# Kernel tuning notes

Hardware: AMD Instinct MI355X
Metric: run time of the kernel (lower is better)

Reference implementation:

```python
import jax, jax.numpy as jnp
import numpy as np

D_MODEL = 256
N_LAYERS = 8
NUM_CLASSES = 3
INPUT_DIM = 1
BATCH = 8
SEQ = 2048
EXIT_IDX = (1, 3, 5, 7)  # n_layers//4-1, n_layers//2-1, 3n//4-1, n-1
LN_EPS = 1e-5


def setup_inputs() -> dict:
    key = jax.random.key(0)
    ks = jax.random.split(key, 16)
    d, nl, nc = D_MODEL, N_LAYERS, NUM_CLASSES
    return {
        "x": jax.random.normal(ks[0], (BATCH, SEQ, INPUT_DIM), jnp.float32),
        "in_W": jax.random.normal(ks[1], (d, INPUT_DIM), jnp.float32) * 0.02,
        "in_b": jnp.zeros((d,), jnp.float32),
        "A_params": jax.random.normal(ks[2], (nl, d), jnp.float32) * 0.1,
        "B_params": jax.random.normal(ks[3], (nl, d), jnp.float32),
        "C_params": jax.random.normal(ks[4], (nl, d), jnp.float32),
        "D_params": jax.random.normal(ks[5], (nl, d), jnp.float32),
        "proj_W": jax.random.normal(ks[6], (nl, d, d), jnp.float32) * 0.02,
        "proj_b": jnp.zeros((nl, d), jnp.float32),
        "ln_g": jnp.ones((nl, d), jnp.float32),
        "ln_b": jnp.zeros((nl, d), jnp.float32),
        "head_W": jax.random.normal(ks[7], (4, nc, d), jnp.float32) * 0.02,
        "head_b": jnp.zeros((4, nc), jnp.float32),
    }


def _ssm_block(x, Ap, Bp, Cp, Dp, pW, pb, g, b):
    # x: [B, L, d]
    Bsz, L, d = x.shape
    A = jax.nn.sigmoid(Ap)                               # [d]
    t = jnp.arange(L, dtype=jnp.float32)
    K = (Cp[:, None] * (A[:, None] ** t[None, :]) * Bp[:, None])[:, None, :]  # [d,1,L]
    xt = jnp.swapaxes(x, 1, 2)                           # [B, d, L]
    # torch F.conv1d(pad=L-1, groups=d) then [..., :L] == left-pad-only cross-correlation
    out = jax.lax.conv_general_dilated(
        xt, K, window_strides=(1,), padding=[(L - 1, 0)], feature_group_count=d
    )                                                    # [B, d, L]
    out = out + Dp[None, :, None] * xt
    out = jnp.swapaxes(out, 1, 2)                        # [B, L, d]
    out = jax.nn.gelu(out, approximate=False) @ pW.T + pb
    y = x + out
    mu = jnp.mean(y, axis=-1, keepdims=True)
    var = jnp.var(y, axis=-1, keepdims=True)
    return (y - mu) / jnp.sqrt(var + LN_EPS) * g + b


def reference(x, in_W, in_b, A_params, B_params, C_params, D_params,
              proj_W, proj_b, ln_g, ln_b, head_W, head_b):
    h = x @ in_W.T + in_b                                # [B, L, d]
    logits = []
    head = 0
    for i in range(N_LAYERS):
        h = _ssm_block(h, A_params[i], B_params[i], C_params[i], D_params[i],
                       proj_W[i], proj_b[i], ln_g[i], ln_b[i])
        if i in EXIT_IDX:
            pooled = jnp.mean(h, axis=1)                 # [B, d]
            logits.append(pooled @ head_W[head].T + head_b[head])
            head += 1
    return jnp.stack(logits, axis=0)                     # [4, B, num_classes]
```

## Files before the change

kernel.cpp:

```cpp
#include <hip/hip_runtime.h>
#include <math.h>

#define DM 256
#define LSEQ 2048
#define BATCH 8
#define NLAYER 8
#define EMAX 192
#define LN_EPS 1e-5f
#define BM 32
#define BLKS 64
#define NPROD 7
#define TAILB 57

#define AL_OFF  16384
#define RED_OFF 32768
#define SMEM_SZ (RED_OFF + 1280)

typedef float f32x4 __attribute__((ext_vector_type(4)));
typedef short bf16x8 __attribute__((ext_vector_type(8)));
typedef unsigned short u16;
typedef unsigned short u16x4 __attribute__((ext_vector_type(4)));
typedef unsigned short u16x8 __attribute__((ext_vector_type(8)));

union V8 { u16x8 u; bf16x8 b; };

__device__ __forceinline__ float erf_fast(float x) {
    float ax = fabsf(x);
    float t = __builtin_amdgcn_rcpf(fmaf(0.3275911f, ax, 1.f));
    float p = fmaf(t, 1.061405429f, -1.453152027f);
    p = fmaf(t, p, 1.421413741f);
    p = fmaf(t, p, -0.284496736f);
    p = fmaf(t, p, 0.254829592f);
    p = p * t;
    float e = __expf(-ax * ax);
    float r = 1.f - p * e;
    return copysignf(r, x);
}

__device__ __forceinline__ float gelu_fast(float v) {
    return 0.5f * v * (1.f + erf_fast(v * 0.70710678118654752f));
}

__device__ __forceinline__ void split2(float g, u16& hi, u16& lo) {
    unsigned u = __float_as_uint(g);
    hi = (u16)(u >> 16);
    float fh = __uint_as_float(u & 0xFFFF0000u);
    float r = g - fh;
    unsigned v = __float_as_uint(r);
    v = v + 0x7FFFu + ((v >> 16) & 1u);
    lo = (u16)(v >> 16);
}

__device__ __forceinline__ int a_addr(int row, int wn, int fr) {
    int unit = wn * 8 + (fr >> 1);
    return row * 512 + ((unit ^ (row & 7)) << 4) + (fr & 1) * 8;
}

__global__ void k_prep(const float* __restrict__ pW, u16* __restrict__ pWh,
                       u16* __restrict__ pWl,
                       const float* __restrict__ x, const float* __restrict__ inW,
                       const float* __restrict__ inb, const float* __restrict__ Ap,
                       const float* __restrict__ Bp, const float* __restrict__ Cp,
                       float* __restrict__ P_all, float* __restrict__ logA_all,
                       float* __restrict__ CB_all, float* __restrict__ pooled,
                       int* __restrict__ flags) {
    if (blockIdx.x < 256) {
        int i = blockIdx.x * 256 + threadIdx.x;
        int e = i * 8;
        int l = e >> 16;
        int r = e & 65535;
        int cg = r >> 12;
        int ks = (r >> 9) & 7;
        int lane = (r >> 3) & 63;
        int fq = lane >> 4, fr = lane & 15;
        int col = (cg >> 2) * 64 + fr * 4 + (cg & 3);
        int k = ks * 32 + fq * 8;
        const float* src = pW + l * 65536 + col * 256 + k;
        float4 w0 = *(const float4*)src;
        float4 w1 = *(const float4*)(src + 4);
        float vv[8] = {w0.x, w0.y, w0.z, w0.w, w1.x, w1.y, w1.z, w1.w};
        u16 sh[8], sl[8];
#pragma unroll
        for (int j = 0; j < 8; ++j) split2(vv[j], sh[j], sl[j]);
        u16x8 vh = {sh[0], sh[1], sh[2], sh[3], sh[4], sh[5], sh[6], sh[7]};
        u16x8 vl = {sl[0], sl[1], sl[2], sl[3], sl[4], sl[5], sl[6], sl[7]};
        *(u16x8*)&pWh[e] = vh;
        *(u16x8*)&pWl[e] = vl;
    } else {
        int b = blockIdx.x - 256;
        int c = threadIdx.x;
        float A0 = 1.f / (1.f + expf(-Ap[c]));
        float iw = inW[c], ib = inb[c];
        const float* xb = x + b * LSEQ;
        float pw = 1.f, acc = 0.f;
        for (int t = 0; t <= EMAX; ++t) {
            acc += (xb[t] * iw + ib) * pw;
            pw *= A0;
        }
        P_all[b * DM + c] = acc;
        for (int l = 1; l < NLAYER; ++l) P_all[l * BATCH * DM + b * DM + c] = 0.f;
        for (int e = 0; e < 4; ++e) pooled[e * BATCH * DM + b * DM + c] = 0.f;
        if (b == 0) {
            for (int l = 0; l < NLAYER; ++l) {
                float Al = 1.f / (1.f + expf(-Ap[l * DM + c]));
                logA_all[l * DM + c] = logf(Al);
                CB_all[l * DM + c]   = Bp[l * DM + c] * Cp[l * DM + c];
            }
            if (c < NLAYER * BATCH) flags[c] = 0;
        }
    }
}

__global__ __launch_bounds__(256, 1) void k_fused(
    const float* __restrict__ x, const float* __restrict__ inW,
    const float* __restrict__ inb,
    const u16* __restrict__ pWh, const u16* __restrict__ pWl,
    const float* __restrict__ Dp_all, const float* __restrict__ pb_all,
    const float* __restrict__ lng_all, const float* __restrict__ lnb_all,
    const float* __restrict__ logA_all, const float* __restrict__ CB_all,
    float* __restrict__ P_all, float* __restrict__ pooled,
    int* __restrict__ flags)
{
    __shared__ __align__(16) char smem[SMEM_SZ];

    int tid  = threadIdx.x;
    int lane = tid & 63;
    int wn   = tid >> 6;
    int fr   = lane & 15;
    int fq   = lane >> 4;

    int b    = blockIdx.x >> 6;
    int blk  = blockIdx.x & 63;
    int brow = b * LSEQ + blk * BM;
    bool isTail = (blk >= TAILB);
    bool isProd = (blk < NPROD);

    int col0 = wn * 64 + fr * 4;
    float hreg[2][4][4];

    {
        float4 wi = *(const float4*)&inW[col0];
        float4 bi = *(const float4*)&inb[col0];
        float4 d0 = *(const float4*)&Dp_all[col0];
        float4 la0, cb0, P0;
        if (isTail) {
            la0 = *(const float4*)&logA_all[col0];
            cb0 = *(const float4*)&CB_all[col0];
            P0  = *(const float4*)&P_all[b * DM + col0];
        }
#pragma unroll
        for (int m = 0; m < 2; ++m)
#pragma unroll
            for (int r = 0; r < 4; ++r) {
                int row = m * 16 + fq * 4 + r;
                int gr  = brow + row;
                float xv = x[gr];
                int u = (LSEQ - 1) - (gr & (LSEQ - 1));
                bool tl = isTail && (u <= EMAX);
                float uf = (float)u;
                float v[4];
                v[0] = fmaf(xv, wi.x, bi.x); hreg[m][0][r] = v[0];
                v[1] = fmaf(xv, wi.y, bi.y); hreg[m][1][r] = v[1];
                v[2] = fmaf(xv, wi.z, bi.z); hreg[m][2][r] = v[2];
                v[3] = fmaf(xv, wi.w, bi.w); hreg[m][3][r] = v[3];
                v[0] *= d0.x; v[1] *= d0.y; v[2] *= d0.z; v[3] *= d0.w;
                if (tl) {
                    v[0] += cb0.x * __expf(uf * la0.x) * P0.x;
                    v[1] += cb0.y * __expf(uf * la0.y) * P0.y;
                    v[2] += cb0.z * __expf(uf * la0.z) * P0.z;
                    v[3] += cb0.w * __expf(uf * la0.w) * P0.w;
                }
                u16 sh[4], sl[4];
#pragma unroll
                for (int n = 0; n < 4; ++n) split2(gelu_fast(v[n]), sh[n], sl[n]);
                u16x4 vh = {sh[0], sh[1], sh[2], sh[3]};
                u16x4 vl = {sl[0], sl[1], sl[2], sl[3]};
                int aby = a_addr(row, wn, fr);
                *(u16x4*)(smem + aby) = vh;
                *(u16x4*)(smem + AL_OFF + aby) = vl;
            }
    }

    V8 bhd[2][4], bld[2][4];
    {
        const u16* bhp0 = pWh + wn * 16384 + lane * 8;
        const u16* blp0 = pWl + wn * 16384 + lane * 8;
#pragma unroll
        for (int n = 0; n < 4; ++n) {
            bhd[0][n].u = *(const u16x8*)&bhp0[n * 4096];
            bld[0][n].u = *(const u16x8*)&blp0[n * 4096];
        }
    }
    __syncthreads();

    for (int l = 0; l < NLAYER; ++l) {
        const u16* bhp = pWh + (size_t)l * 65536 + wn * 16384 + lane * 8;
        const u16* blp = pWl + (size_t)l * 65536 + wn * 16384 + lane * 8;

        f32x4 acc[2][4];
#pragma unroll
        for (int m = 0; m < 2; ++m)
#pragma unroll
            for (int n = 0; n < 4; ++n) acc[m][n] = (f32x4){0.f, 0.f, 0.f, 0.f};

#pragma unroll
        for (int ks = 0; ks < 8; ++ks) {
            int cur = ks & 1, nxt = cur ^ 1;
            if (ks < 7) {
#pragma unroll
                for (int n = 0; n < 4; ++n) {
                    bhd[nxt][n].u = *(const u16x8*)&bhp[n * 4096 + (ks + 1) * 512];
                    bld[nxt][n].u = *(const u16x8*)&blp[n * 4096 + (ks + 1) * 512];
                }
            }
            V8 ah[2], al[2];
#pragma unroll
            for (int m = 0; m < 2; ++m) {
                int row = m * 16 + fr;
                int aby = row * 512 + (((ks * 4 + fq) ^ (row & 7)) << 4);
                ah[m].u = *(const u16x8*)(smem + aby);
                al[m].u = *(const u16x8*)(smem + AL_OFF + aby);
            }
#pragma unroll
            for (int m = 0; m < 2; ++m)
#pragma unroll
                for (int n = 0; n < 4; ++n) {
                    acc[m][n] = __builtin_amdgcn_mfma_f32_16x16x32_bf16(ah[m].b, bhd[cur][n].b, acc[m][n], 0, 0, 0);
                    acc[m][n] = __builtin_amdgcn_mfma_f32_16x16x32_bf16(ah[m].b, bld[cur][n].b, acc[m][n], 0, 0, 0);
                    acc[m][n] = __builtin_amdgcn_mfma_f32_16x16x32_bf16(al[m].b, bhd[cur][n].b, acc[m][n], 0, 0, 0);
                }
        }

        float4 pbv = *(const float4*)&pb_all[l * DM + col0];
        float4 lgv = *(const float4*)&lng_all[l * DM + col0];
        float4 lbv = *(const float4*)&lnb_all[l * DM + col0];
        float s[2][4], ss[2][4];
#pragma unroll
        for (int m = 0; m < 2; ++m)
#pragma unroll
            for (int r = 0; r < 4; ++r) {
                float y0 = hreg[m][0][r] + acc[m][0][r] + pbv.x;
                float y1 = hreg[m][1][r] + acc[m][1][r] + pbv.y;
                float y2 = hreg[m][2][r] + acc[m][2][r] + pbv.z;
                float y3 = hreg[m][3][r] + acc[m][3][r] + pbv.w;
                acc[m][0][r] = y0; acc[m][1][r] = y1;
                acc[m][2][r] = y2; acc[m][3][r] = y3;
                s[m][r]  = y0 + y1 + y2 + y3;
                ss[m][r] = y0 * y0 + y1 * y1 + y2 * y2 + y3 * y3;
            }
#pragma unroll
        for (int m = 0; m < 2; ++m)
#pragma unroll
            for (int r = 0; r < 4; ++r)
#pragma unroll
                for (int msk = 1; msk < 16; msk <<= 1) {
                    s[m][r]  += __shfl_xor(s[m][r],  msk);
                    ss[m][r] += __shfl_xor(ss[m][r], msk);
                }
        if (fr == 0) {
#pragma unroll
            for (int m = 0; m < 2; ++m)
#pragma unroll
                for (int r = 0; r < 4; ++r) {
                    int row = m * 16 + fq * 4 + r;
                    *(float*)(smem + RED_OFF + (row * 10 + wn * 2)     * 4) = s[m][r];
                    *(float*)(smem + RED_OFF + (row * 10 + wn * 2 + 1) * 4) = ss[m][r];
                }
        }
        __syncthreads();

        float mean[2][4], rstd[2][4];
#pragma unroll
        for (int m = 0; m < 2; ++m)
#pragma unroll
            for (int r = 0; r < 4; ++r) {
                int row = m * 16 + fq * 4 + r;
                float st = 0.f, sst = 0.f;
#pragma unroll
                for (int w = 0; w < 4; ++w) {
                    st  += *(const float*)(smem + RED_OFF + (row * 10 + w * 2)     * 4);
                    sst += *(const float*)(smem + RED_OFF + (row * 10 + w * 2 + 1) * 4);
                }
                float mu = st * (1.f / 256.f);
                float var = sst * (1.f / 256.f) - mu * mu;
                mean[m][r] = mu;
                rstd[m][r] = rsqrtf(var + LN_EPS);
            }
        int slot = (l == 1) ? 0 : (l == 3) ? 1 : (l == 5) ? 2 : (l == 7) ? 3 : -1;
        bool last = (l == NLAYER - 1);
        bool prod = !last && isProd;
        float4 Dnv, lanv;
        if (!last) Dnv = *(const float4*)&Dp_all[(l + 1) * DM + col0];
        if (prod)  lanv = *(const float4*)&logA_all[(l + 1) * DM + col0];
        float cs[4] = {0.f, 0.f, 0.f, 0.f};
        float pc[4] = {0.f, 0.f, 0.f, 0.f};
#pragma unroll
        for (int m = 0; m < 2; ++m)
#pragma unroll
            for (int r = 0; r < 4; ++r) {
                int row  = m * 16 + fq * 4 + r;
                int trow = blk * BM + row;
                float o0 = (acc[m][0][r] - mean[m][r]) * rstd[m][r] * lgv.x + lbv.x;
                float o1 = (acc[m][1][r] - mean[m][r]) * rstd[m][r] * lgv.y + lbv.y;
                float o2 = (acc[m][2][r] - mean[m][r]) * rstd[m][r] * lgv.z + lbv.z;
                float o3 = (acc[m][3][r] - mean[m][r]) * rstd[m][r] * lgv.w + lbv.w;
                hreg[m][0][r] = o0; hreg[m][1][r] = o1;
                hreg[m][2][r] = o2; hreg[m][3][r] = o3;
                if (slot >= 0) { cs[0] += o0; cs[1] += o1; cs[2] += o2; cs[3] += o3; }
                if (prod && trow <= EMAX) {
                    float tf = (float)trow;
                    pc[0] += o0 * __expf(tf * lanv.x);
                    pc[1] += o1 * __expf(tf * lanv.y);
                    pc[2] += o2 * __expf(tf * lanv.z);
                    pc[3] += o3 * __expf(tf * lanv.w);
                }
                if (!last) {
                    u16 sh[4], sl[4];
                    split2(gelu_fast(Dnv.x * o0), sh[0], sl[0]);
                    split2(gelu_fast(Dnv.y * o1), sh[1], sl[1]);
                    split2(gelu_fast(Dnv.z * o2), sh[2], sl[2]);
                    split2(gelu_fast(Dnv.w * o3), sh[3], sl[3]);
                    u16x4 vh = {sh[0], sh[1], sh[2], sh[3]};
                    u16x4 vl = {sl[0], sl[1], sl[2], sl[3]};
                    int aby = a_addr(row, wn, fr);
                    *(u16x4*)(smem + aby) = vh;
                    *(u16x4*)(smem + AL_OFF + aby) = vl;
                }
            }
        if (slot >= 0) {
#pragma unroll
            for (int n = 0; n < 4; ++n) {
                cs[n] += __shfl_xor(cs[n], 16);
                cs[n] += __shfl_xor(cs[n], 32);
            }
            if (lane < 16) {
#pragma unroll
                for (int n = 0; n < 4; ++n)
                    atomicAdd(&pooled[slot * (BATCH * DM) + b * DM + wn * 64 + lane * 4 + n], cs[n]);
            }
        }
        if (prod) {
#pragma unroll
            for (int n = 0; n < 4; ++n) {
                pc[n] += __shfl_xor(pc[n], 16);
                pc[n] += __shfl_xor(pc[n], 32);
            }
            if (lane < 16) {
#pragma unroll
                for (int n = 0; n < 4; ++n)
                    atomicAdd(&P_all[(size_t)(l + 1) * BATCH * DM + b * DM + wn * 64 + lane * 4 + n], pc[n]);
            }
        }

        if (!last) {
            const u16* bhpN = pWh + (size_t)(l + 1) * 65536 + wn * 16384 + lane * 8;
            const u16* blpN = pWl + (size_t)(l + 1) * 65536 + wn * 16384 + lane * 8;
#pragma unroll
            for (int n = 0; n < 4; ++n) {
                bhd[0][n].u = *(const u16x8*)&bhpN[n * 4096];
                bld[0][n].u = *(const u16x8*)&blpN[n * 4096];
            }
        }
        __syncthreads();

        if (!last) {
            if (prod && tid == 0)
                __hip_atomic_fetch_add(&flags[(l + 1) * BATCH + b], 1,
                                       __ATOMIC_RELEASE, __HIP_MEMORY_SCOPE_AGENT);
            if (isTail) {
                if (tid == 0) {
                    while (__hip_atomic_load(&flags[(l + 1) * BATCH + b], __ATOMIC_ACQUIRE,
                                             __HIP_MEMORY_SCOPE_AGENT) < NPROD)
                        __builtin_amdgcn_s_sleep(2);
                }
                __syncthreads();
                float4 lanx = *(const float4*)&logA_all[(l + 1) * DM + col0];
                float4 cbnx = *(const float4*)&CB_all[(l + 1) * DM + col0];
                float Pn[4];
#pragma unroll
                for (int n = 0; n < 4; ++n)
                    Pn[n] = __hip_atomic_load(
                        &P_all[(size_t)(l + 1) * BATCH * DM + b * DM + col0 + n],
                        __ATOMIC_RELAXED, __HIP_MEMORY_SCOPE_AGENT);
                float lan[4] = {lanx.x, lanx.y, lanx.z, lanx.w};
                float cbn[4] = {cbnx.x, cbnx.y, cbnx.z, cbnx.w};
                float Dn[4]  = {Dnv.x, Dnv.y, Dnv.z, Dnv.w};
#pragma unroll
                for (int m = 0; m < 2; ++m)
#pragma unroll
                    for (int r = 0; r < 4; ++r) {
                        int row = m * 16 + fq * 4 + r;
                        int u = (LSEQ - 1) - ((brow + row) & (LSEQ - 1));
                        if (u <= EMAX) {
                            float uf = (float)u;
                            u16 sh[4], sl[4];
#pragma unroll
                            for (int n = 0; n < 4; ++n) {
                                float v = Dn[n] * hreg[m][n][r] +
                                          cbn[n] * __expf(uf * lan[n]) * Pn[n];
                                split2(gelu_fast(v), sh[n], sl[n]);
                            }
                            u16x4 vh = {sh[0], sh[1], sh[2], sh[3]};
                            u16x4 vl = {sl[0], sl[1], sl[2], sl[3]};
                            int aby = a_addr(row, wn, fr);
                            *(u16x4*)(smem + aby) = vh;
                            *(u16x4*)(smem + AL_OFF + aby) = vl;
                        }
                    }
                __syncthreads();
            }
        }
    }
}

__global__ void k_head(const float* __restrict__ pooled, const float* __restrict__ hW,
                       const float* __restrict__ hb, float* __restrict__ out) {
    int tid = threadIdx.x;
    if (tid >= 96) return;
    int e = tid / 24;
    int r = tid % 24;
    int b = r / 3;
    int n = r % 3;
    const float* pv = &pooled[e * (BATCH * DM) + b * DM];
    const float* wv = &hW[(e * 3 + n) * DM];
    float acc = 0.f;
    for (int c = 0; c < DM; ++c) acc += pv[c] * wv[c];
    out[e * 24 + b * 3 + n] = acc * (1.f / (float)LSEQ) + hb[e * 3 + n];
}

extern "C" void kernel_launch(void* const* d_in, const int* in_sizes, int n_in,
                              void* d_out, int out_size, void* d_ws, size_t ws_size,
                              hipStream_t stream) {
    const float* x   = (const float*)d_in[0];
    const float* inW = (const float*)d_in[1];
    const float* inb = (const float*)d_in[2];
    const float* Ap  = (const float*)d_in[3];
    const float* Bp  = (const float*)d_in[4];
    const float* Cp  = (const float*)d_in[5];
    const float* Dp  = (const float*)d_in[6];
    const float* pW  = (const float*)d_in[7];
    const float* pb  = (const float*)d_in[8];
    const float* lng = (const float*)d_in[9];
    const float* lnb = (const float*)d_in[10];
    const float* hW  = (const float*)d_in[11];
    const float* hb  = (const float*)d_in[12];
    float* out = (float*)d_out;

    float* ws = (float*)d_ws;
    float* P_all    = ws;
    float* logA_all = P_all + NLAYER * BATCH * DM;
    float* CB_all   = logA_all + NLAYER * DM;
    float* pooled   = CB_all + NLAYER * DM;
    u16* pWh        = (u16*)(pooled + 4 * BATCH * DM);
    u16* pWl        = pWh + NLAYER * DM * DM;
    int* flags      = (int*)(pWl + NLAYER * DM * DM);

    k_prep<<<264, 256, 0, stream>>>(pW, pWh, pWl, x, inW, inb, Ap, Bp, Cp,
                                    P_all, logA_all, CB_all, pooled, flags);
    k_fused<<<BATCH * BLKS, 256, 0, stream>>>(
        x, inW, inb, pWh, pWl, Dp, pb, lng, lnb,
        logA_all, CB_all, P_all, pooled, flags);
    k_head<<<1, 128, 0, stream>>>(pooled, hW, hb, out);
}
```

Before: 126.8 us.

## Split fused SSM kernel across 8 waves with 32 columns each

Doubles the block size of the fused layer kernel from 256 to 512 threads, so each wave owns 32 output columns instead of 64. The pre-split weight layout, the swizzled LDS address mapping and the LayerNorm cross-wave reduction buffer are all reworked to match. The aim is more waves per CU to hide the latency of the MFMA chain and the weight loads while cutting per-thread registers. The cost is a wider LayerNorm reduction (8 partials per row), narrower LDS stores, and more waves contending at each barrier.

```diff
diff --git a/kernel.cpp b/kernel.cpp
--- a/kernel.cpp
+++ b/kernel.cpp
@@ -14,12 +14,12 @@
 
 #define AL_OFF  16384
 #define RED_OFF 32768
-#define SMEM_SZ (RED_OFF + 1280)
+#define SMEM_SZ (RED_OFF + 2304)
 
 typedef float f32x4 __attribute__((ext_vector_type(4)));
 typedef short bf16x8 __attribute__((ext_vector_type(8)));
 typedef unsigned short u16;
-typedef unsigned short u16x4 __attribute__((ext_vector_type(4)));
+typedef unsigned short u16x2 __attribute__((ext_vector_type(2)));
 typedef unsigned short u16x8 __attribute__((ext_vector_type(8)));
 
 union V8 { u16x8 u; bf16x8 b; };
@@ -52,8 +52,8 @@
 }
 
 __device__ __forceinline__ int a_addr(int row, int wn, int fr) {
-    int unit = wn * 8 + (fr >> 1);
-    return row * 512 + ((unit ^ (row & 7)) << 4) + (fr & 1) * 8;
+    int unit = wn * 4 + (fr >> 2);
+    return row * 512 + ((unit ^ (row & 7)) << 4) + (fr & 3) * 4;
 }
 
 __global__ void k_prep(const float* __restrict__ pW, u16* __restrict__ pWh,
@@ -73,7 +73,7 @@
         int ks = (r >> 9) & 7;
         int lane = (r >> 3) & 63;
         int fq = lane >> 4, fr = lane & 15;
-        int col = (cg >> 2) * 64 + fr * 4 + (cg & 3);
+        int col = (cg >> 1) * 32 + fr * 2 + (cg & 1);
         int k = ks * 32 + fq * 8;
         const float* src = pW + l * 65536 + col * 256 + k;
         float4 w0 = *(const float4*)src;
@@ -111,7 +111,7 @@
     }
 }
 
-__global__ __launch_bounds__(256, 1) void k_fused(
+__global__ __launch_bounds__(512, 1) void k_fused(
     const float* __restrict__ x, const float* __restrict__ inW,
     const float* __restrict__ inb,
     const u16* __restrict__ pWh, const u16* __restrict__ pWl,
@@ -135,18 +135,19 @@
     bool isTail = (blk >= TAILB);
     bool isProd = (blk < NPROD);
 
-    int col0 = wn * 64 + fr * 4;
-    float hreg[2][4][4];
+    int col0 = wn * 32 + fr * 2;
+    float hreg[2][2][4];
+    float* Pbuf = (float*)(smem + RED_OFF);
 
     {
-        float4 wi = *(const float4*)&inW[col0];
-        float4 bi = *(const float4*)&inb[col0];
-        float4 d0 = *(const float4*)&Dp_all[col0];
-        float4 la0, cb0, P0;
+        float2 wi = *(const float2*)&inW[col0];
+        float2 bi = *(const float2*)&inb[col0];
+        float2 d0 = *(const float2*)&Dp_all[col0];
+        float2 la0, cb0, P0;
         if (isTail) {
-            la0 = *(const float4*)&logA_all[col0];
-            cb0 = *(const float4*)&CB_all[col0];
-            P0  = *(const float4*)&P_all[b * DM + col0];
+            la0 = *(const float2*)&logA_all[col0];
+            cb0 = *(const float2*)&CB_all[col0];
+            P0  = *(const float2*)&P_all[b * DM + col0];
         }
 #pragma unroll
         for (int m = 0; m < 2; ++m)
@@ -158,35 +159,30 @@
                 int u = (LSEQ - 1) - (gr & (LSEQ - 1));
                 bool tl = isTail && (u <= EMAX);
                 float uf = (float)u;
-                float v[4];
-                v[0] = fmaf(xv, wi.x, bi.x); hreg[m][0][r] = v[0];
-                v[1] = fmaf(xv, wi.y, bi.y); hreg[m][1][r] = v[1];
-                v[2] = fmaf(xv, wi.z, bi.z); hreg[m][2][r] = v[2];
-                v[3] = fmaf(xv, wi.w, bi.w); hreg[m][3][r] = v[3];
-                v[0] *= d0.x; v[1] *= d0.y; v[2] *= d0.z; v[3] *= d0.w;
+                float v0 = fmaf(xv, wi.x, bi.x); hreg[m][0][r] = v0;
+                float v1 = fmaf(xv, wi.y, bi.y); hreg[m][1][r] = v1;
+                v0 *= d0.x; v1 *= d0.y;
                 if (tl) {
-                    v[0] += cb0.x * __expf(uf * la0.x) * P0.x;
-                    v[1] += cb0.y * __expf(uf * la0.y) * P0.y;
-                    v[2] += cb0.z * __expf(uf * la0.z) * P0.z;
-                    v[3] += cb0.w * __expf(uf * la0.w) * P0.w;
-                }
-                u16 sh[4], sl[4];
-#pragma unroll
-                for (int n = 0; n < 4; ++n) split2(gelu_fast(v[n]), sh[n], sl[n]);
-                u16x4 vh = {sh[0], sh[1], sh[2], sh[3]};
-                u16x4 vl = {sl[0], sl[1], sl[2], sl[3]};
+                    v0 += cb0.x * __expf(uf * la0.x) * P0.x;
+                    v1 += cb0.y * __expf(uf * la0.y) * P0.y;
+                }
+                u16 h0, l0, h1, l1;
+                split2(gelu_fast(v0), h0, l0);
+                split2(gelu_fast(v1), h1, l1);
+                u16x2 vh = {h0, h1};
+                u16x2 vl = {l0, l1};
                 int aby = a_addr(row, wn, fr);
-                *(u16x4*)(smem + aby) = vh;
-                *(u16x4*)(smem + AL_OFF + aby) = vl;
+                *(u16x2*)(smem + aby) = vh;
+                *(u16x2*)(smem + AL_OFF + aby) = vl;
             }
     }
 
-    V8 bhd[2][4], bld[2][4];
+    V8 bhd[2][2], bld[2][2];
     {
-        const u16* bhp0 = pWh + wn * 16384 + lane * 8;
-        const u16* blp0 = pWl + wn * 16384 + lane * 8;
-#pragma unroll
-        for (int n = 0; n < 4; ++n) {
+        const u16* bhp0 = pWh + wn * 8192 + lane * 8;
+        const u16* blp0 = pWl + wn * 8192 + lane * 8;
+#pragma unroll
+        for (int n = 0; n < 2; ++n) {
             bhd[0][n].u = *(const u16x8*)&bhp0[n * 4096];
             bld[0][n].u = *(const u16x8*)&blp0[n * 4096];
         }
@@ -194,21 +190,21 @@
     __syncthreads();
 
     for (int l = 0; l < NLAYER; ++l) {
-        const u16* bhp = pWh + (size_t)l * 65536 + wn * 16384 + lane * 8;
-        const u16* blp = pWl + (size_t)l * 65536 + wn * 16384 + lane * 8;
-
-        f32x4 acc[2][4];
-#pragma unroll
-        for (int m = 0; m < 2; ++m)
-#pragma unroll
-            for (int n = 0; n < 4; ++n) acc[m][n] = (f32x4){0.f, 0.f, 0.f, 0.f};
+        const u16* bhp = pWh + (size_t)l * 65536 + wn * 8192 + lane * 8;
+        const u16* blp = pWl + (size_t)l * 65536 + wn * 8192 + lane * 8;
+
+        f32x4 acc[2][2];
+#pragma unroll
+        for (int m = 0; m < 2; ++m)
+#pragma unroll
+            for (int n = 0; n < 2; ++n) acc[m][n] = (f32x4){0.f, 0.f, 0.f, 0.f};
 
 #pragma unroll
         for (int ks = 0; ks < 8; ++ks) {
             int cur = ks & 1, nxt = cur ^ 1;
             if (ks < 7) {
 #pragma unroll
-                for (int n = 0; n < 4; ++n) {
+                for (int n = 0; n < 2; ++n) {
                     bhd[nxt][n].u = *(const u16x8*)&bhp[n * 4096 + (ks + 1) * 512];
                     bld[nxt][n].u = *(const u16x8*)&blp[n * 4096 + (ks + 1) * 512];
                 }
@@ -224,16 +220,16 @@
 #pragma unroll
             for (int m = 0; m < 2; ++m)
 #pragma unroll
-                for (int n = 0; n < 4; ++n) {
+                for (int n = 0; n < 2; ++n) {
                     acc[m][n] = __builtin_amdgcn_mfma_f32_16x16x32_bf16(ah[m].b, bhd[cur][n].b, acc[m][n], 0, 0, 0);
                     acc[m][n] = __builtin_amdgcn_mfma_f32_16x16x32_bf16(ah[m].b, bld[cur][n].b, acc[m][n], 0, 0, 0);
                     acc[m][n] = __builtin_amdgcn_mfma_f32_16x16x32_bf16(al[m].b, bhd[cur][n].b, acc[m][n], 0, 0, 0);
                 }
         }
 
-        float4 pbv = *(const float4*)&pb_all[l * DM + col0];
-        float4 lgv = *(const float4*)&lng_all[l * DM + col0];
-        float4 lbv = *(const float4*)&lnb_all[l * DM + col0];
+        float2 pbv = *(const float2*)&pb_all[l * DM + col0];
+        float2 lgv = *(const float2*)&lng_all[l * DM + col0];
+        float2 lbv = *(const float2*)&lnb_all[l * DM + col0];
         float s[2][4], ss[2][4];
 #pragma unroll
         for (int m = 0; m < 2; ++m)
@@ -241,12 +237,9 @@
             for (int r = 0; r < 4; ++r) {
                 float y0 = hreg[m][0][r] + acc[m][0][r] + pbv.x;
                 float y1 = hreg[m][1][r] + acc[m][1][r] + pbv.y;
-                float y2 = hreg[m][2][r] + acc[m][2][r] + pbv.z;
-                float y3 = hreg[m][3][r] + acc[m][3][r] + pbv.w;
                 acc[m][0][r] = y0; acc[m][1][r] = y1;
-                acc[m][2][r] = y2; acc[m][3][r] = y3;
-                s[m][r]  = y0 + y1 + y2 + y3;
-                ss[m][r] = y0 * y0 + y1 * y1 + y2 * y2 + y3 * y3;
+                s[m][r]  = y0 + y1;
+                ss[m][r] = y0 * y0 + y1 * y1;
             }
 #pragma unroll
         for (int m = 0; m < 2; ++m)
@@ -263,8 +256,8 @@
 #pragma unroll
                 for (int r = 0; r < 4; ++r) {
                     int row = m * 16 + fq * 4 + r;
-                    *(float*)(smem + RED_OFF + (row * 10 + wn * 2)     * 4) = s[m][r];
-                    *(float*)(smem + RED_OFF + (row * 10 + wn * 2 + 1) * 4) = ss[m][r];
+                    *(float*)(smem + RED_OFF + (row * 18 + wn * 2)     * 4) = s[m][r];
+                    *(float*)(smem + RED_OFF + (row * 18 + wn * 2 + 1) * 4) = ss[m][r];
                 }
         }
         __syncthreads();
@@ -277,9 +270,9 @@
                 int row = m * 16 + fq * 4 + r;
                 float st = 0.f, sst = 0.f;
 #pragma unroll
-                for (int w = 0; w < 4; ++w) {
-                    st  += *(const float*)(smem + RED_OFF + (row * 10 + w * 2)     * 4);
-                    sst += *(const float*)(smem + RED_OFF + (row * 10 + w * 2 + 1) * 4);
+                for (int w = 0; w < 8; ++w) {
+                    st  += *(const float*)(smem + RED_OFF + (row * 18 + w * 2)     * 4);
+                    sst += *(const float*)(smem + RED_OFF + (row * 18 + w * 2 + 1) * 4);
                 }
                 float mu = st * (1.f / 256.f);
                 float var = sst * (1.f / 256.f) - mu * mu;
@@ -289,11 +282,11 @@
         int slot = (l == 1) ? 0 : (l == 3) ? 1 : (l == 5) ? 2 : (l == 7) ? 3 : -1;
         bool last = (l == NLAYER - 1);
         bool prod = !last && isProd;
-        float4 Dnv, lanv;
-        if (!last) Dnv = *(const float4*)&Dp_all[(l + 1) * DM + col0];
-        if (prod)  lanv = *(const float4*)&logA_all[(l + 1) * DM + col0];
-        float cs[4] = {0.f, 0.f, 0.f, 0.f};
-        float pc[4] = {0.f, 0.f, 0.f, 0.f};
+        float2 Dnv, lanv;
+        if (!last) Dnv = *(const float2*)&Dp_all[(l + 1) * DM + col0];
+        if (prod)  lanv = *(const float2*)&logA_all[(l + 1) * DM + col0];
+        float cs[2] = {0.f, 0.f};
+        float pc[2] = {0.f, 0.f};
 #pragma unroll
         for (int m = 0; m < 2; ++m)
 #pragma unroll
@@ -302,61 +295,54 @@
                 int trow = blk * BM + row;
                 float o0 = (acc[m][0][r] - mean[m][r]) * rstd[m][r] * lgv.x + lbv.x;
                 float o1 = (acc[m][1][r] - mean[m][r]) * rstd[m][r] * lgv.y + lbv.y;
-                float o2 = (acc[m][2][r] - mean[m][r]) * rstd[m][r] * lgv.z + lbv.z;
-                float o3 = (acc[m][3][r] - mean[m][r]) * rstd[m][r] * lgv.w + lbv.w;
                 hreg[m][0][r] = o0; hreg[m][1][r] = o1;
-                hreg[m][2][r] = o2; hreg[m][3][r] = o3;
-                if (slot >= 0) { cs[0] += o0; cs[1] += o1; cs[2] += o2; cs[3] += o3; }
+                if (slot >= 0) { cs[0] += o0; cs[1] += o1; }
                 if (prod && trow <= EMAX) {
                     float tf = (float)trow;
                     pc[0] += o0 * __expf(tf * lanv.x);
                     pc[1] += o1 * __expf(tf * lanv.y);
-                    pc[2] += o2 * __expf(tf * lanv.z);
-                    pc[3] += o3 * __expf(tf * lanv.w);
                 }
                 if (!last) {
-                    u16 sh[4], sl[4];
-                    split2(gelu_fast(Dnv.x * o0), sh[0], sl[0]);
-                    split2(gelu_fast(Dnv.y * o1), sh[1], sl[1]);
-                    split2(gelu_fast(Dnv.z * o2), sh[2], sl[2]);
-                    split2(gelu_fast(Dnv.w * o3), sh[3], sl[3]);
-                    u16x4 vh = {sh[0], sh[1], sh[2], sh[3]};
-                    u16x4 vl = {sl[0], sl[1], sl[2], sl[3]};
+                    u16 h0, l0, h1, l1;
+                    split2(gelu_fast(Dnv.x * o0), h0, l0);
+                    split2(gelu_fast(Dnv.y * o1), h1, l1);
+                    u16x2 vh = {h0, h1};
+                    u16x2 vl = {l0, l1};
                     int aby = a_addr(row, wn, fr);
-                    *(u16x4*)(smem + aby) = vh;
-                    *(u16x4*)(smem + AL_OFF + aby) = vl;
+                    *(u16x2*)(smem + aby) = vh;
+                    *(u16x2*)(smem + AL_OFF + aby) = vl;
                 }
             }
         if (slot >= 0) {
 #pragma unroll
-            for (int n = 0; n < 4; ++n) {
+            for (int n = 0; n < 2; ++n) {
                 cs[n] += __shfl_xor(cs[n], 16);
                 cs[n] += __shfl_xor(cs[n], 32);
             }
             if (lane < 16) {
 #pragma unroll
-                for (int n = 0; n < 4; ++n)
-                    atomicAdd(&pooled[slot * (BATCH * DM) + b * DM + wn * 64 + lane * 4 + n], cs[n]);
+                for (int n = 0; n < 2; ++n)
+                    atomicAdd(&pooled[slot * (BATCH * DM) + b * DM + wn * 32 + lane * 2 + n], cs[n]);
             }
         }
         if (prod) {
 #pragma unroll
-            for (int n = 0; n < 4; ++n) {
+            for (int n = 0; n < 2; ++n) {
                 pc[n] += __shfl_xor(pc[n], 16);
                 pc[n] += __shfl_xor(pc[n], 32);
             }
             if (lane < 16) {
 #pragma unroll
-                for (int n = 0; n < 4; ++n)
-                    atomicAdd(&P_all[(size_t)(l + 1) * BATCH * DM + b * DM + wn * 64 + lane * 4 + n], pc[n]);
+                for (int n = 0; n < 2; ++n)
+                    atomicAdd(&P_all[(size_t)(l + 1) * BATCH * DM + b * DM + wn * 32 + lane * 2 + n], pc[n]);
             }
         }
 
         if (!last) {
-            const u16* bhpN = pWh + (size_t)(l + 1) * 65536 + wn * 16384 + lane * 8;
-            const u16* blpN = pWl + (size_t)(l + 1) * 65536 + wn * 16384 + lane * 8;
-#pragma unroll
-            for (int n = 0; n < 4; ++n) {
+            const u16* bhpN = pWh + (size_t)(l + 1) * 65536 + wn * 8192 + lane * 8;
+            const u16* blpN = pWl + (size_t)(l + 1) * 65536 + wn * 8192 + lane * 8;
+#pragma unroll
+            for (int n = 0; n < 2; ++n) {
                 bhd[0][n].u = *(const u16x8*)&bhpN[n * 4096];
                 bld[0][n].u = *(const u16x8*)&blpN[n * 4096];
             }
@@ -374,17 +360,17 @@
                         __builtin_amdgcn_s_sleep(2);
                 }
                 __syncthreads();
-                float4 lanx = *(const float4*)&logA_all[(l + 1) * DM + col0];
-                float4 cbnx = *(const float4*)&CB_all[(l + 1) * DM + col0];
-                float Pn[4];
-#pragma unroll
-                for (int n = 0; n < 4; ++n)
+                float2 lanx = *(const float2*)&logA_all[(l + 1) * DM + col0];
+                float2 cbnx = *(const float2*)&CB_all[(l + 1) * DM + col0];
+                float Pn[2];
+#pragma unroll
+                for (int n = 0; n < 2; ++n)
                     Pn[n] = __hip_atomic_load(
                         &P_all[(size_t)(l + 1) * BATCH * DM + b * DM + col0 + n],
                         __ATOMIC_RELAXED, __HIP_MEMORY_SCOPE_AGENT);
-                float lan[4] = {lanx.x, lanx.y, lanx.z, lanx.w};
-                float cbn[4] = {cbnx.x, cbnx.y, cbnx.z, cbnx.w};
-                float Dn[4]  = {Dnv.x, Dnv.y, Dnv.z, Dnv.w};
+                float lan[2] = {lanx.x, lanx.y};
+                float cbn[2] = {cbnx.x, cbnx.y};
+                float Dn[2]  = {Dnv.x, Dnv.y};
 #pragma unroll
                 for (int m = 0; m < 2; ++m)
 #pragma unroll
@@ -393,18 +379,16 @@
                         int u = (LSEQ - 1) - ((brow + row) & (LSEQ - 1));
                         if (u <= EMAX) {
                             float uf = (float)u;
-                            u16 sh[4], sl[4];
-#pragma unroll
-                            for (int n = 0; n < 4; ++n) {
-                                float v = Dn[n] * hreg[m][n][r] +
-                                          cbn[n] * __expf(uf * lan[n]) * Pn[n];
-                                split2(gelu_fast(v), sh[n], sl[n]);
-                            }
-                            u16x4 vh = {sh[0], sh[1], sh[2], sh[3]};
-                            u16x4 vl = {sl[0], sl[1], sl[2], sl[3]};
+                            u16 h0, l0, h1, l1;
+                            float v0 = Dn[0] * hreg[m][0][r] + cbn[0] * __expf(uf * lan[0]) * Pn[0];
+                            float v1 = Dn[1] * hreg[m][1][r] + cbn[1] * __expf(uf * lan[1]) * Pn[1];
+                            split2(gelu_fast(v0), h0, l0);
+                            split2(gelu_fast(v1), h1, l1);
+                            u16x2 vh = {h0, h1};
+                            u16x2 vl = {l0, l1};
                             int aby = a_addr(row, wn, fr);
-                            *(u16x4*)(smem + aby) = vh;
-                            *(u16x4*)(smem + AL_OFF + aby) = vl;
+                            *(u16x2*)(smem + aby) = vh;
+                            *(u16x2*)(smem + AL_OFF + aby) = vl;
                         }
                     }
                 __syncthreads();
@@ -457,7 +441,7 @@
 
     k_prep<<<264, 256, 0, stream>>>(pW, pWh, pWl, x, inW, inb, Ap, Bp, Cp,
                                     P_all, logA_all, CB_all, pooled, flags);
-    k_fused<<<BATCH * BLKS, 256, 0, stream>>>(
+    k_fused<<<BATCH * BLKS, 512, 0, stream>>>(
         x, inW, inb, pWh, pWl, Dp, pb, lng, lnb,
         logA_all, CB_all, P_all, pooled, flags);
     k_head<<<1, 128, 0, stream>>>(pooled, hW, hb, out);
```

New measurement: 162.7 us. +28.3%, slower.
